# Optimization experiments

Measured on AMD Instinct MI355X. Metric: run time of the kernel, lower is better.

## Reference

```python
import jax, jax.numpy as jnp
import numpy as np

N_NODES = 50000
N_EDGES = 1000000


def _edge_conv(x, src, dst, W, b, n_nodes):
    """PyG EdgeConv: msg = nn(cat([x_i, x_j - x_i])), aggr=max over incoming edges."""
    xi = x[dst]                      # [E, C] target features
    xj = x[src]                      # [E, C] source features
    m = jnp.concatenate([xi, xj - xi], axis=-1)          # [E, 2C]
    m = jax.nn.relu(m @ W + b)                           # [E, C_out]
    out = jax.ops.segment_max(m, dst, num_segments=n_nodes)  # [N, C_out]
    # empty segments produce -inf; PyG fills with 0
    return jnp.where(jnp.isfinite(out), out, 0.0)


def setup_inputs() -> dict:
    key = jax.random.key(0)
    ks = jax.random.split(key, 12)
    x = jax.random.normal(ks[0], (N_NODES, 3), dtype=jnp.float32)
    edge_index = jax.random.randint(ks[1], (2, N_EDGES), 0, N_NODES, dtype=jnp.int64)

    def lin(k, fan_in, fan_out):
        s = 1.0 / np.sqrt(fan_in)
        kw, kb = jax.random.split(k)
        W = jax.random.uniform(kw, (fan_in, fan_out), jnp.float32, -s, s)
        b = jax.random.uniform(kb, (fan_out,), jnp.float32, -s, s)
        return W, b

    W1, b1 = lin(ks[2], 6, 64)       # conv1 MLP([3*2, 64])
    W2, b2 = lin(ks[3], 128, 128)    # conv2 MLP([64*2, 128])
    W3, b3 = lin(ks[4], 256, 512)    # conv3 MLP([128*2, 512])
    W4, b4 = lin(ks[5], 512, 256)    # lin1 MLP([512, 256])
    W5, b5 = lin(ks[6], 256, 3)      # lin1 final Linear(256, 3)
    return {"x": x, "edge_index": edge_index,
            "W1": W1, "b1": b1, "W2": W2, "b2": b2, "W3": W3, "b3": b3,
            "W4": W4, "b4": b4, "W5": W5, "b5": b5}


def reference(x, edge_index, W1, b1, W2, b2, W3, b3, W4, b4, W5, b5):
    src = edge_index[0]  # x_j
    dst = edge_index[1]  # x_i (aggregation target)
    n = x.shape[0]
    x1 = _edge_conv(x, src, dst, W1, b1, n)    # [N, 64]
    x2 = _edge_conv(x1, src, dst, W2, b2, n)   # [N, 128]
    x3 = _edge_conv(x2, src, dst, W3, b3, n)   # [N, 512]
    x4 = jax.nn.relu(x3 @ W4 + b4) @ W5 + b5   # [N, 3]
    return x + x4
```

## Files before the change

kernel.cpp:

```cpp
#include <hip/hip_runtime.h>

static constexpr int NN = 50000;
static constexpr int NE = 1000000;

typedef short bf16x8 __attribute__((ext_vector_type(8)));
typedef float f32x4 __attribute__((ext_vector_type(4)));
typedef unsigned short u16x2 __attribute__((ext_vector_type(2)));

__device__ inline float bf2f_raw(unsigned short u) {
    return __uint_as_float(((unsigned int)u) << 16);
}
__device__ inline unsigned short f2bf(float f) {
    unsigned int u = __float_as_uint(f);
    u += 0x7fffu + ((u >> 16) & 1u);
    return (unsigned short)(u >> 16);
}
__device__ inline unsigned short f2bfs(float f) {
    unsigned short b = f2bf(f);
    return (b & 0x8000u) ? (unsigned short)(~b) : (unsigned short)(b | 0x8000u);
}
__device__ inline float unsrt2f(unsigned short v) {
    unsigned short b = (v & 0x8000u) ? (unsigned short)(v ^ 0x8000u)
                                     : (unsigned short)(~v);
    return bf2f_raw(b);
}
__device__ inline unsigned int pkmax(unsigned int a, unsigned int b) {
    u16x2 r = __builtin_elementwise_max(__builtin_bit_cast(u16x2, a),
                                        __builtin_bit_cast(u16x2, b));
    return __builtin_bit_cast(unsigned int, r);
}
__device__ inline uint4 pkmax4(uint4 a, uint4 b) {
    a.x = pkmax(a.x, b.x); a.y = pkmax(a.y, b.y);
    a.z = pkmax(a.z, b.z); a.w = pkmax(a.w, b.w);
    return a;
}
__device__ inline unsigned int pack2(float f0, float f1) {
    return (unsigned int)f2bf(f0) | ((unsigned int)f2bf(f1) << 16);
}
__device__ inline unsigned int addrelu2t(unsigned int a, unsigned int t) {
    float t0 = unsrt2f((unsigned short)(t & 0xffffu));
    float t1 = unsrt2f((unsigned short)(t >> 16));
    float f0 = fmaxf(bf2f_raw((unsigned short)(a & 0xffffu)) + t0, 0.f);
    float f1 = fmaxf(bf2f_raw((unsigned short)(a >> 16)) + t1, 0.f);
    return pack2(f0, f1);
}


__global__ void setup_kernel(const float* __restrict__ x, const float* __restrict__ W1,
                             const float* __restrict__ b1, const float* __restrict__ b5,
                             const float* __restrict__ W2, const float* __restrict__ W3,
                             const float* __restrict__ W4,
                             unsigned short* __restrict__ as1, float* __restrict__ out,
                             int* __restrict__ deg, int* __restrict__ cursor,
                             unsigned short* __restrict__ Bt2,
                             unsigned short* __restrict__ Bt3,
                             unsigned short* __restrict__ W4t) {
    int t = blockIdx.x * blockDim.x + threadIdx.x;
    if (t < NN * 128) {
        int i = t >> 7, c = t & 127;
        float x0 = x[i * 3 + 0], x1 = x[i * 3 + 1], x2 = x[i * 3 + 2];
        if (c < 64) {
            float v = x0 * (W1[c] - W1[192 + c]) + x1 * (W1[64 + c] - W1[256 + c]) +
                      x2 * (W1[128 + c] - W1[320 + c]) + b1[c];
            as1[t] = f2bf(v);
        } else {
            int cs = c - 64;
            float v = x0 * W1[192 + cs] + x1 * W1[256 + cs] + x2 * W1[320 + cs];
            as1[t] = f2bfs(v);
        }
        return;
    }
    t -= NN * 128;
    if (t < NN * 3) { out[t] = x[t] + b5[t % 3]; return; }
    t -= NN * 3;
    if (t < NN) { deg[t] = 0; return; }
    t -= NN;
    if (t < NN) { cursor[t] = 0; return; }
    t -= NN;
    if (t < 8192) {
        int k = t / 128, c = t % 128;
        float wt = W2[k * 128 + c];
        float wb = W2[(64 + k) * 128 + c];
        Bt2[c * 64 + k] = f2bf(wt - wb);
        Bt2[(128 + c) * 64 + k] = f2bf(wb);
        return;
    }
    t -= 8192;
    if (t < 65536) {
        int k = t / 512, c = t % 512;
        float wt = W3[k * 512 + c];
        float wb = W3[(128 + k) * 512 + c];
        Bt3[c * 128 + k] = f2bf(wt - wb);
        Bt3[(512 + c) * 128 + k] = f2bf(wb);
        return;
    }
    t -= 65536;
    if (t < 131072) {
        int k = t / 256, n = t % 256;
        W4t[n * 512 + k] = f2bf(W4[k * 256 + n]);
    }
}


__global__ void hist_kernel(const int* __restrict__ dst, int* __restrict__ deg) {
    int e = blockIdx.x * blockDim.x + threadIdx.x;
    if (e < NE) atomicAdd(&deg[dst[e]], 1);
}

__global__ __launch_bounds__(1024) void scan_kernel(const int* __restrict__ deg,
                                                    int* __restrict__ rowstart) {
    __shared__ int wave_sums[16];
    constexpr int CH = (NN + 1023) / 1024;
    int tid = threadIdx.x;
    int lane = tid & 63;
    int wave = tid >> 6;
    int base = tid * CH;
    int vals[CH];
    int sum = 0;
    #pragma unroll
    for (int i = 0; i < CH; ++i) {
        int idx = base + i;
        vals[i] = (idx < NN) ? deg[idx] : 0;
        sum += vals[i];
    }
    int x = sum;
    #pragma unroll
    for (int off = 1; off < 64; off <<= 1) {
        int y = __shfl_up(x, off);
        if (lane >= off) x += y;
    }
    if (lane == 63) wave_sums[wave] = x;
    __syncthreads();
    if (wave == 0 && lane < 16) {
        int s = wave_sums[lane];
        #pragma unroll
        for (int off = 1; off < 16; off <<= 1) {
            int y = __shfl_up(s, off);
            if (lane >= off) s += y;
        }
        wave_sums[lane] = s;
    }
    __syncthreads();
    int run = (wave ? wave_sums[wave - 1] : 0) + x - sum;
    #pragma unroll
    for (int i = 0; i < CH; ++i) {
        int idx = base + i;
        if (idx < NN) rowstart[idx] = run;
        run += vals[i];
    }
    if (tid == 1023) rowstart[NN] = run;
}

__global__ void scatter_kernel(const int* __restrict__ src, const int* __restrict__ dst,
                               const int* __restrict__ rowstart, int* __restrict__ cursor,
                               int* __restrict__ csr) {
    int e = blockIdx.x * blockDim.x + threadIdx.x;
    if (e < NE) {
        int d = dst[e];
        int pos = atomicAdd(&cursor[d], 1);
        csr[rowstart[d] + pos] = src[e];
    }
}


__global__ __launch_bounds__(256) void edge_fused_conv1_kernel(
    const unsigned short* __restrict__ as, const int* __restrict__ rowstart,
    const int* __restrict__ csr, unsigned short* __restrict__ x1) {
    int wid = (blockIdx.x * 256 + threadIdx.x) >> 6;
    int lane = threadIdx.x & 63;
    if (wid >= NN) return;
    int e0 = __builtin_amdgcn_readfirstlane(rowstart[wid]);
    int e1 = __builtin_amdgcn_readfirstlane(rowstart[wid + 1]);
    int nedge = e1 - e0;
    unsigned int mA = 0u, mB = 0u;
    if (nedge > 0) {
        int last = nedge - 1;
        for (int e = 0; e < nedge; e += 16) {
            int jj[16];
            #pragma unroll
            for (int k = 0; k < 16; ++k) {
                int idx = e + k; if (idx > last) idx = last;
                jj[k] = __builtin_amdgcn_readfirstlane(csr[e0 + idx]);
            }
            unsigned int v[16];
            #pragma unroll
            for (int k = 0; k < 16; ++k)
                v[k] = *(const unsigned short*)(as + (size_t)jj[k] * 128 + 64 + lane);
            #pragma unroll
            for (int k = 0; k < 16; ++k) {
                if (k & 1) mB = mB > v[k] ? mB : v[k];
                else       mA = mA > v[k] ? mA : v[k];
            }
        }
    }
    unsigned int m = mA > mB ? mA : mB;
    unsigned short a = as[(size_t)wid * 128 + lane];
    float t = unsrt2f((unsigned short)m);
    float f = fmaxf(bf2f_raw(a) + t, 0.f);
    x1[(size_t)wid * 64 + lane] = f2bf(f);
}


__global__ __launch_bounds__(256) void ef128_a2_kernel(
    const unsigned short* __restrict__ s2, const unsigned short* __restrict__ x1,
    const int* __restrict__ rowstart, const int* __restrict__ csr,
    const unsigned short* __restrict__ Bt2a, const float* __restrict__ b2,
    unsigned short* __restrict__ x2) {
    __shared__ __align__(16) unsigned short x1t[16][72];
    __shared__ __align__(16) unsigned short A2[16][136];
    int tid = threadIdx.x;
    int wave = tid >> 6, lane = tid & 63;
    int quad = lane >> 4, l16 = lane & 15;
    int tilebase = blockIdx.x * 16;

    if (tid < 128) {
        int row = tid >> 3, seg = tid & 7;
        uint4 v = *(const uint4*)(x1 + (size_t)(tilebase + row) * 64 + seg * 8);
        *(uint4*)&x1t[row][seg * 8] = v;
    }
    __syncthreads();

    unsigned int m[4];
    for (int i = 0; i < 4; ++i) {
        int node = tilebase + wave * 4 + i;
        int e0 = __builtin_amdgcn_readfirstlane(rowstart[node]);
        int e1 = __builtin_amdgcn_readfirstlane(rowstart[node + 1]);
        int nedge = e1 - e0;
        unsigned int mA = 0u, mB = 0u;
        if (nedge > 0) {
            int last = nedge - 1;
            for (int e = 0; e < nedge; e += 16) {
                int jj[16];
                #pragma unroll
                for (int k = 0; k < 16; ++k) {
                    int idx = e + k; if (idx > last) idx = last;
                    jj[k] = __builtin_amdgcn_readfirstlane(csr[e0 + idx]);
                }
                unsigned int v[16];
                #pragma unroll
                for (int k = 0; k < 16; ++k)
                    v[k] = *(const unsigned int*)(s2 + (size_t)jj[k] * 128 + lane * 2);
                #pragma unroll
                for (int k = 0; k < 16; ++k) {
                    if (k & 1) mB = pkmax(mB, v[k]);
                    else       mA = pkmax(mA, v[k]);
                }
            }
        }
        m[i] = pkmax(mA, mB);
    }

    {
        int colbase = wave * 32;
        f32x4 acc[2] = {};
        #pragma unroll
        for (int kc = 0; kc < 2; ++kc) {
            bf16x8 afr = *(const bf16x8*)&x1t[l16][kc * 32 + quad * 8];
            #pragma unroll
            for (int nt = 0; nt < 2; ++nt) {
                int col = colbase + nt * 16 + l16;
                bf16x8 bfr = *(const bf16x8*)&Bt2a[(size_t)col * 64 + kc * 32 + quad * 8];
                acc[nt] = __builtin_amdgcn_mfma_f32_16x16x32_bf16(afr, bfr, acc[nt], 0, 0, 0);
            }
        }
        #pragma unroll
        for (int nt = 0; nt < 2; ++nt) {
            int col = colbase + nt * 16 + l16;
            float bv = b2[col];
            #pragma unroll
            for (int r = 0; r < 4; ++r)
                A2[quad * 4 + r][col] = f2bf(acc[nt][r] + bv);
        }
    }
    __syncthreads();

    #pragma unroll
    for (int i = 0; i < 4; ++i) {
        int row = wave * 4 + i;
        unsigned int av = *(const unsigned int*)&A2[row][lane * 2];
        *(unsigned int*)(x2 + (size_t)(tilebase + row) * 128 + lane * 2) =
            addrelu2t(av, m[i]);
    }
}


__global__ __launch_bounds__(256) void ef512_w5_kernel(
    const unsigned short* __restrict__ s3, const unsigned short* __restrict__ x2,
    const int* __restrict__ rowstart, const int* __restrict__ csr,
    const unsigned short* __restrict__ Bt3a, const float* __restrict__ b3,
    const unsigned short* __restrict__ W4t,
    const float* __restrict__ b4, const float* __restrict__ W5,
    float* __restrict__ out) {
    __shared__ __align__(16) unsigned short X[16][520];
    int tid = threadIdx.x;
    int wave = tid >> 6, lane = tid & 63;
    int quad = lane >> 4, l16 = lane & 15;
    int tilebase = blockIdx.x * 16;

    {
        int row = tid >> 4, seg = tid & 15;
        uint4 v = *(const uint4*)(x2 + (size_t)(tilebase + row) * 128 + seg * 8);
        *(uint4*)&X[row][seg * 8] = v;
    }
    __syncthreads();
    bf16x8 afr[4];
    #pragma unroll
    for (int kc = 0; kc < 4; ++kc)
        afr[kc] = *(const bf16x8*)&X[l16][kc * 32 + quad * 8];
    __syncthreads();

    uint4 m[4];
    for (int i = 0; i < 4; ++i) {
        int node = tilebase + wave * 4 + i;
        int e0 = __builtin_amdgcn_readfirstlane(rowstart[node]);
        int e1 = __builtin_amdgcn_readfirstlane(rowstart[node + 1]);
        int nedge = e1 - e0;
        uint4 mA = make_uint4(0u, 0u, 0u, 0u), mB = make_uint4(0u, 0u, 0u, 0u);
        if (nedge > 0) {
            int last = nedge - 1;
            for (int e = 0; e < nedge; e += 8) {
                int jj[8];
                #pragma unroll
                for (int k = 0; k < 8; ++k) {
                    int idx = e + k; if (idx > last) idx = last;
                    jj[k] = __builtin_amdgcn_readfirstlane(csr[e0 + idx]);
                }
                uint4 v[8];
                #pragma unroll
                for (int k = 0; k < 8; ++k)
                    v[k] = *(const uint4*)(s3 + (size_t)jj[k] * 512 + lane * 8);
                #pragma unroll
                for (int k = 0; k < 8; ++k) {
                    if (k & 1) mB = pkmax4(mB, v[k]);
                    else       mA = pkmax4(mA, v[k]);
                }
            }
        }
        m[i] = pkmax4(mA, mB);
    }

    {
        int colbase = wave * 128;
        f32x4 acc3[8] = {};
        #pragma unroll
        for (int kc = 0; kc < 4; ++kc) {
            #pragma unroll
            for (int nt = 0; nt < 8; ++nt) {
                int col = colbase + nt * 16 + l16;
                bf16x8 bfr = *(const bf16x8*)&Bt3a[(size_t)col * 128 + kc * 32 + quad * 8];
                acc3[nt] = __builtin_amdgcn_mfma_f32_16x16x32_bf16(afr[kc], bfr, acc3[nt], 0, 0, 0);
            }
        }
        #pragma unroll
        for (int nt = 0; nt < 8; ++nt) {
            int col = colbase + nt * 16 + l16;
            float bv = b3[col];
            #pragma unroll
            for (int r = 0; r < 4; ++r)
                X[quad * 4 + r][col] = f2bf(acc3[nt][r] + bv);
        }
    }
    __syncthreads();

    #pragma unroll
    for (int i = 0; i < 4; ++i) {
        int row = wave * 4 + i;
        uint4 av = *(const uint4*)&X[row][lane * 8];
        uint4 o;
        o.x = addrelu2t(av.x, m[i].x);
        o.y = addrelu2t(av.y, m[i].y);
        o.z = addrelu2t(av.z, m[i].z);
        o.w = addrelu2t(av.w, m[i].w);
        *(uint4*)&X[row][lane * 8] = o;
    }
    __syncthreads();

    int colbase = wave * 64;
    f32x4 acc4[4] = {};
    for (int kc = 0; kc < 16; ++kc) {
        bf16x8 a4 = *(const bf16x8*)&X[l16][kc * 32 + quad * 8];
        #pragma unroll
        for (int nt = 0; nt < 4; ++nt) {
            int col = colbase + nt * 16 + l16;
            bf16x8 bfr = *(const bf16x8*)&W4t[(size_t)col * 512 + kc * 32 + quad * 8];
            acc4[nt] = __builtin_amdgcn_mfma_f32_16x16x32_bf16(a4, bfr, acc4[nt], 0, 0, 0);
        }
    }
    float b4v[4], w5r[4][3];
    #pragma unroll
    for (int nt = 0; nt < 4; ++nt) {
        int col = colbase + nt * 16 + l16;
        b4v[nt] = b4[col];
        w5r[nt][0] = W5[col * 3 + 0];
        w5r[nt][1] = W5[col * 3 + 1];
        w5r[nt][2] = W5[col * 3 + 2];
    }
    #pragma unroll
    for (int r = 0; r < 4; ++r) {
        int row = tilebase + quad * 4 + r;
        float p0 = 0.f, p1 = 0.f, p2 = 0.f;
        #pragma unroll
        for (int nt = 0; nt < 4; ++nt) {
            float h = fmaxf(acc4[nt][r] + b4v[nt], 0.f);
            p0 += h * w5r[nt][0];
            p1 += h * w5r[nt][1];
            p2 += h * w5r[nt][2];
        }
        #pragma unroll
        for (int mm = 8; mm; mm >>= 1) {
            p0 += __shfl_xor(p0, mm);
            p1 += __shfl_xor(p1, mm);
            p2 += __shfl_xor(p2, mm);
        }
        if (l16 == 0) {
            atomicAdd(&out[row * 3 + 0], p0);
            atomicAdd(&out[row * 3 + 1], p1);
            atomicAdd(&out[row * 3 + 2], p2);
        }
    }
}


template<int K, int NT>
__global__ __launch_bounds__(256) void mfma_gemm_nloop_kernel(
    const unsigned short* __restrict__ A, const unsigned short* __restrict__ Bt,
    const float* __restrict__ bias, int bias_n,
    unsigned short* __restrict__ C, int M) {
    constexpr int KC = K / 32;
    constexpr int N = NT * 128;
    __shared__ __align__(16) unsigned short Asl[KC][128 * 40];
    __shared__ __align__(16) unsigned short Bsl[128 * 40];
    int tid = threadIdx.x;
    int mbase = blockIdx.x * 128;
    int wave = tid >> 6, lane = tid & 63;
    int wm = (wave >> 1) * 64, wn = (wave & 1) * 64;
    int quad = lane >> 4, l16 = lane & 15;

    #pragma unroll
    for (int c = tid; c < KC * 512; c += 256) {
        int kc = c >> 9, rem = c & 511;
        int r = rem >> 2, kk = (rem & 3) * 8;
        uint4 va = make_uint4(0u, 0u, 0u, 0u);
        int gr = mbase + r;
        if (gr < M) va = *(const uint4*)&A[(size_t)gr * K + kc * 32 + kk];
        *(uint4*)&Asl[kc][r * 40 + kk] = va;
    }

    for (int nt = 0; nt < NT; ++nt) {
        int nbase = nt * 128;
        f32x4 acc[4][4] = {};
        for (int kc = 0; kc < KC; ++kc) {
            __syncthreads();
            #pragma unroll
            for (int h = 0; h < 2; ++h) {
                int c = tid + h * 256;
                int r = c >> 2, kk = (c & 3) * 8;
                uint4 vb = *(const uint4*)&Bt[(size_t)(nbase + r) * K + kc * 32 + kk];
                *(uint4*)&Bsl[r * 40 + kk] = vb;
            }
            __syncthreads();
            bf16x8 af[4], bfr[4];
            #pragma unroll
            for (int tt = 0; tt < 4; ++tt) {
                af[tt]  = *(const bf16x8*)&Asl[kc][(wm + tt * 16 + l16) * 40 + quad * 8];
                bfr[tt] = *(const bf16x8*)&Bsl[(wn + tt * 16 + l16) * 40 + quad * 8];
            }
            #pragma unroll
            for (int mt = 0; mt < 4; ++mt)
                #pragma unroll
                for (int ntt = 0; ntt < 4; ++ntt)
                    acc[mt][ntt] = __builtin_amdgcn_mfma_f32_16x16x32_bf16(
                        af[mt], bfr[ntt], acc[mt][ntt], 0, 0, 0);
        }
        #pragma unroll
        for (int mt = 0; mt < 4; ++mt) {
            #pragma unroll
            for (int r = 0; r < 4; ++r) {
                int row = mbase + wm + mt * 16 + quad * 4 + r;
                if (row >= M) continue;
                #pragma unroll
                for (int ntt = 0; ntt < 4; ++ntt) {
                    int col = nbase + wn + ntt * 16 + l16;
                    float v = acc[mt][ntt][r];
                    unsigned short o;
                    if (col < bias_n) o = f2bf(v + bias[col]);
                    else o = f2bfs(v);
                    C[(size_t)row * N + col] = o;
                }
            }
        }
    }
}

__global__ void fallback_copy_kernel(const float* __restrict__ x, float* __restrict__ out) {
    int t = blockIdx.x * blockDim.x + threadIdx.x;
    if (t < NN * 3) out[t] = x[t];
}


extern "C" void kernel_launch(void* const* d_in, const int* in_sizes, int n_in,
                              void* d_out, int out_size, void* d_ws, size_t ws_size,
                              hipStream_t stream) {
    const float* x  = (const float*)d_in[0];
    const int*   ei = (const int*)d_in[1];
    const float* W1 = (const float*)d_in[2];
    const float* b1 = (const float*)d_in[3];
    const float* W2 = (const float*)d_in[4];
    const float* b2 = (const float*)d_in[5];
    const float* W3 = (const float*)d_in[6];
    const float* b3 = (const float*)d_in[7];
    const float* W4 = (const float*)d_in[8];
    const float* b4 = (const float*)d_in[9];
    const float* W5 = (const float*)d_in[10];
    const float* b5 = (const float*)d_in[11];
    float* out = (float*)d_out;

    char* p = (char*)d_ws;
    auto alloc = [&](size_t bytes) -> void* {
        void* r = (void*)p;
        p += (bytes + 255) & ~(size_t)255;
        return r;
    };
    int* deg      = (int*)alloc((size_t)NN * 4);
    int* rowstart = (int*)alloc((size_t)(NN + 1) * 4);
    int* cursor   = (int*)alloc((size_t)NN * 4);
    int* csr      = (int*)alloc((size_t)NE * 4);
    unsigned short* Bt2 = (unsigned short*)alloc(256 * 64 * 2);
    unsigned short* Bt3 = (unsigned short*)alloc(1024 * 128 * 2);
    unsigned short* W4t = (unsigned short*)alloc(256 * 512 * 2);
    unsigned short* x1 = (unsigned short*)alloc((size_t)NN * 64 * 2);
    unsigned short* x2 = (unsigned short*)alloc((size_t)NN * 128 * 2);
    unsigned short* as_slab = (unsigned short*)alloc((size_t)NN * 512 * 2);
    size_t need = (size_t)(p - (char*)d_ws);
    if (ws_size < need) {
        fallback_copy_kernel<<<(NN * 3 + 255) / 256, 256, 0, stream>>>(x, out);
        return;
    }

    const int* src = ei;
    const int* dst = ei + NE;

    constexpr int SETUP_T = NN * 128 + NN * 3 + NN + NN + 8192 + 65536 + 131072;
    setup_kernel<<<(SETUP_T + 255) / 256, 256, 0, stream>>>(
        x, W1, b1, b5, W2, W3, W4, as_slab, out, deg, cursor, Bt2, Bt3, W4t);

    hist_kernel<<<(NE + 255) / 256, 256, 0, stream>>>(dst, deg);
    scan_kernel<<<1, 1024, 0, stream>>>(deg, rowstart);
    scatter_kernel<<<(NE + 255) / 256, 256, 0, stream>>>(src, dst, rowstart, cursor, csr);

    edge_fused_conv1_kernel<<<12500, 256, 0, stream>>>(as_slab, rowstart, csr, x1);

    mfma_gemm_nloop_kernel<64, 1><<<391, 256, 0, stream>>>(
        x1, Bt2 + 128 * 64, b2, 0, as_slab, NN);
    ef128_a2_kernel<<<NN / 16, 256, 0, stream>>>(
        as_slab, x1, rowstart, csr, Bt2, b2, x2);

    mfma_gemm_nloop_kernel<128, 4><<<391, 256, 0, stream>>>(
        x2, Bt3 + 512 * 128, b3, 0, as_slab, NN);

    ef512_w5_kernel<<<NN / 16, 256, 0, stream>>>(
        as_slab, x2, rowstart, csr, Bt3, b3, W4t, b4, W5, out);
}
```

Baseline: 579.0 us.

## Compute per-edge source transforms on the fly for conv1 and conv2

Conv1 no longer precomputes a per-node source-transform slab. Each wave loads the raw 3-float coordinates of its neighbours, shares them via shuffles, and evaluates the 3-term dot product inline. Conv2 drops its separate source GEMM kernel: it gathers 64-wide x1 neighbour rows into shared memory, runs MFMA per 16-edge batch, and max-reduces into a shared sortable-bf16 buffer. This trades the slab writes and gather bandwidth for recomputed per-edge GEMMs (16x more MFMA work in conv2) and extra LDS traffic. The conv3 kernel also moves its self-GEMM ahead of the neighbour gather.

```diff
diff --git a/kernel.cpp b/kernel.cpp
--- a/kernel.cpp
+++ b/kernel.cpp
@@ -50,27 +50,21 @@
                              const float* __restrict__ b1, const float* __restrict__ b5,
                              const float* __restrict__ W2, const float* __restrict__ W3,
                              const float* __restrict__ W4,
-                             unsigned short* __restrict__ as1, float* __restrict__ out,
+                             unsigned short* __restrict__ a1buf, float* __restrict__ out,
                              int* __restrict__ deg, int* __restrict__ cursor,
                              unsigned short* __restrict__ Bt2,
                              unsigned short* __restrict__ Bt3,
                              unsigned short* __restrict__ W4t) {
     int t = blockIdx.x * blockDim.x + threadIdx.x;
-    if (t < NN * 128) {
-        int i = t >> 7, c = t & 127;
+    if (t < NN * 64) {
+        int i = t >> 6, c = t & 63;
         float x0 = x[i * 3 + 0], x1 = x[i * 3 + 1], x2 = x[i * 3 + 2];
-        if (c < 64) {
-            float v = x0 * (W1[c] - W1[192 + c]) + x1 * (W1[64 + c] - W1[256 + c]) +
-                      x2 * (W1[128 + c] - W1[320 + c]) + b1[c];
-            as1[t] = f2bf(v);
-        } else {
-            int cs = c - 64;
-            float v = x0 * W1[192 + cs] + x1 * W1[256 + cs] + x2 * W1[320 + cs];
-            as1[t] = f2bfs(v);
-        }
+        float v = x0 * (W1[c] - W1[192 + c]) + x1 * (W1[64 + c] - W1[256 + c]) +
+                  x2 * (W1[128 + c] - W1[320 + c]) + b1[c];
+        a1buf[t] = f2bf(v);
         return;
     }
-    t -= NN * 128;
+    t -= NN * 64;
     if (t < NN * 3) { out[t] = x[t] + b5[t % 3]; return; }
     t -= NN * 3;
     if (t < NN) { deg[t] = 0; return; }
@@ -163,51 +157,50 @@
 }
 
 
-__global__ __launch_bounds__(256) void edge_fused_conv1_kernel(
-    const unsigned short* __restrict__ as, const int* __restrict__ rowstart,
-    const int* __restrict__ csr, unsigned short* __restrict__ x1) {
+__global__ __launch_bounds__(256) void conv1_kernel(
+    const float* __restrict__ x, const int* __restrict__ rowstart,
+    const int* __restrict__ csr, const float* __restrict__ W1,
+    const unsigned short* __restrict__ a1buf, unsigned short* __restrict__ x1) {
     int wid = (blockIdx.x * 256 + threadIdx.x) >> 6;
     int lane = threadIdx.x & 63;
     if (wid >= NN) return;
     int e0 = __builtin_amdgcn_readfirstlane(rowstart[wid]);
     int e1 = __builtin_amdgcn_readfirstlane(rowstart[wid + 1]);
-    int nedge = e1 - e0;
-    unsigned int mA = 0u, mB = 0u;
-    if (nedge > 0) {
-        int last = nedge - 1;
-        for (int e = 0; e < nedge; e += 16) {
-            int jj[16];
+    int ne = e1 - e0;
+    float wa = W1[192 + lane], wb = W1[256 + lane], wc = W1[320 + lane];
+    float m = -INFINITY;
+    if (ne > 0) {
+        int last = ne - 1;
+        int eidx = lane >> 2, comp = lane & 3;
+        for (int e = 0; e < ne; e += 16) {
+            int idx = e + eidx; if (idx > last) idx = last;
+            int j = csr[e0 + idx];
+            float v = 0.f;
+            if (comp < 3) v = x[(size_t)j * 3 + comp];
             #pragma unroll
             for (int k = 0; k < 16; ++k) {
-                int idx = e + k; if (idx > last) idx = last;
-                jj[k] = __builtin_amdgcn_readfirstlane(csr[e0 + idx]);
-            }
-            unsigned int v[16];
-            #pragma unroll
-            for (int k = 0; k < 16; ++k)
-                v[k] = *(const unsigned short*)(as + (size_t)jj[k] * 128 + 64 + lane);
-            #pragma unroll
-            for (int k = 0; k < 16; ++k) {
-                if (k & 1) mB = mB > v[k] ? mB : v[k];
-                else       mA = mA > v[k] ? mA : v[k];
-            }
-        }
-    }
-    unsigned int m = mA > mB ? mA : mB;
-    unsigned short a = as[(size_t)wid * 128 + lane];
-    float t = unsrt2f((unsigned short)m);
-    float f = fmaxf(bf2f_raw(a) + t, 0.f);
-    x1[(size_t)wid * 64 + lane] = f2bf(f);
-}
-
-
-__global__ __launch_bounds__(256) void ef128_a2_kernel(
-    const unsigned short* __restrict__ s2, const unsigned short* __restrict__ x1,
-    const int* __restrict__ rowstart, const int* __restrict__ csr,
-    const unsigned short* __restrict__ Bt2a, const float* __restrict__ b2,
-    unsigned short* __restrict__ x2) {
+                float x0 = __shfl(v, k * 4 + 0);
+                float x1v = __shfl(v, k * 4 + 1);
+                float x2v = __shfl(v, k * 4 + 2);
+                float s = x0 * wa + x1v * wb + x2v * wc;
+                s = bf2f_raw(f2bf(s));
+                m = fmaxf(m, s);
+            }
+        }
+    }
+    float a = bf2f_raw(a1buf[(size_t)wid * 64 + lane]);
+    x1[(size_t)wid * 64 + lane] = f2bf(fmaxf(a + m, 0.f));
+}
+
+
+__global__ __launch_bounds__(256) void ef128_x1_kernel(
+    const unsigned short* __restrict__ x1, const int* __restrict__ rowstart,
+    const int* __restrict__ csr, const unsigned short* __restrict__ Bt2,
+    const float* __restrict__ b2, unsigned short* __restrict__ x2) {
     __shared__ __align__(16) unsigned short x1t[16][72];
     __shared__ __align__(16) unsigned short A2[16][136];
+    __shared__ __align__(16) unsigned short M[16][136];
+    __shared__ __align__(16) unsigned short E[4][16][72];
     int tid = threadIdx.x;
     int wave = tid >> 6, lane = tid & 63;
     int quad = lane >> 4, l16 = lane & 15;
@@ -218,37 +211,12 @@
         uint4 v = *(const uint4*)(x1 + (size_t)(tilebase + row) * 64 + seg * 8);
         *(uint4*)&x1t[row][seg * 8] = v;
     }
-    __syncthreads();
-
-    unsigned int m[4];
-    for (int i = 0; i < 4; ++i) {
-        int node = tilebase + wave * 4 + i;
-        int e0 = __builtin_amdgcn_readfirstlane(rowstart[node]);
-        int e1 = __builtin_amdgcn_readfirstlane(rowstart[node + 1]);
-        int nedge = e1 - e0;
-        unsigned int mA = 0u, mB = 0u;
-        if (nedge > 0) {
-            int last = nedge - 1;
-            for (int e = 0; e < nedge; e += 16) {
-                int jj[16];
-                #pragma unroll
-                for (int k = 0; k < 16; ++k) {
-                    int idx = e + k; if (idx > last) idx = last;
-                    jj[k] = __builtin_amdgcn_readfirstlane(csr[e0 + idx]);
-                }
-                unsigned int v[16];
-                #pragma unroll
-                for (int k = 0; k < 16; ++k)
-                    v[k] = *(const unsigned int*)(s2 + (size_t)jj[k] * 128 + lane * 2);
-                #pragma unroll
-                for (int k = 0; k < 16; ++k) {
-                    if (k & 1) mB = pkmax(mB, v[k]);
-                    else       mA = pkmax(mA, v[k]);
-                }
-            }
-        }
-        m[i] = pkmax(mA, mB);
-    }
+    #pragma unroll
+    for (int idx = tid; idx < 16 * 64; idx += 256) {
+        int row = idx >> 6, c2 = idx & 63;
+        *(unsigned int*)&M[row][c2 * 2] = 0u;
+    }
+    __syncthreads();
 
     {
         int colbase = wave * 32;
@@ -259,7 +227,7 @@
             #pragma unroll
             for (int nt = 0; nt < 2; ++nt) {
                 int col = colbase + nt * 16 + l16;
-                bf16x8 bfr = *(const bf16x8*)&Bt2a[(size_t)col * 64 + kc * 32 + quad * 8];
+                bf16x8 bfr = *(const bf16x8*)&Bt2[(size_t)col * 64 + kc * 32 + quad * 8];
                 acc[nt] = __builtin_amdgcn_mfma_f32_16x16x32_bf16(afr, bfr, acc[nt], 0, 0, 0);
             }
         }
@@ -272,14 +240,68 @@
                 A2[quad * 4 + r][col] = f2bf(acc[nt][r] + bv);
         }
     }
+
+    for (int i = 0; i < 4; ++i) {
+        int nl = wave * 4 + i;
+        int node = tilebase + nl;
+        int e0 = __builtin_amdgcn_readfirstlane(rowstart[node]);
+        int e1 = __builtin_amdgcn_readfirstlane(rowstart[node + 1]);
+        int ne = e1 - e0;
+        if (ne <= 0) continue;
+        int last = ne - 1;
+        for (int e = 0; e < ne; e += 16) {
+            int cj[8];
+            #pragma unroll
+            for (int sub = 0; sub < 8; ++sub) {
+                int ee = sub * 2 + (lane >> 5);
+                int idx = e + ee; if (idx > last) idx = last;
+                cj[sub] = csr[e0 + idx];
+            }
+            unsigned int g[8];
+            #pragma unroll
+            for (int sub = 0; sub < 8; ++sub)
+                g[sub] = *(const unsigned int*)(x1 + (size_t)cj[sub] * 64 + (lane & 31) * 2);
+            #pragma unroll
+            for (int sub = 0; sub < 8; ++sub)
+                *(unsigned int*)&E[wave][sub * 2 + (lane >> 5)][(lane & 31) * 2] = g[sub];
+            #pragma unroll
+            for (int half = 0; half < 2; ++half) {
+                f32x4 acc[4] = {};
+                #pragma unroll
+                for (int kc = 0; kc < 2; ++kc) {
+                    bf16x8 afr = *(const bf16x8*)&E[wave][l16][kc * 32 + quad * 8];
+                    #pragma unroll
+                    for (int nt = 0; nt < 4; ++nt) {
+                        int col = half * 64 + nt * 16 + l16;
+                        bf16x8 bfr = *(const bf16x8*)&Bt2[(size_t)(128 + col) * 64 + kc * 32 + quad * 8];
+                        acc[nt] = __builtin_amdgcn_mfma_f32_16x16x32_bf16(afr, bfr, acc[nt], 0, 0, 0);
+                    }
+                }
+                #pragma unroll
+                for (int nt = 0; nt < 4; ++nt) {
+                    float cm = fmaxf(fmaxf(acc[nt][0], acc[nt][1]),
+                                     fmaxf(acc[nt][2], acc[nt][3]));
+                    cm = fmaxf(cm, __shfl_xor(cm, 16));
+                    cm = fmaxf(cm, __shfl_xor(cm, 32));
+                    if (lane < 16) {
+                        unsigned short sv = f2bfs(cm);
+                        int col = half * 64 + nt * 16 + l16;
+                        unsigned short old = M[nl][col];
+                        if (sv > old) M[nl][col] = sv;
+                    }
+                }
+            }
+        }
+    }
     __syncthreads();
 
     #pragma unroll
     for (int i = 0; i < 4; ++i) {
         int row = wave * 4 + i;
         unsigned int av = *(const unsigned int*)&A2[row][lane * 2];
+        unsigned int mv = *(const unsigned int*)&M[row][lane * 2];
         *(unsigned int*)(x2 + (size_t)(tilebase + row) * 128 + lane * 2) =
-            addrelu2t(av, m[i]);
+            addrelu2t(av, mv);
     }
 }
 
@@ -309,6 +331,28 @@
         afr[kc] = *(const bf16x8*)&X[l16][kc * 32 + quad * 8];
     __syncthreads();
 
+    {
+        int colbase = wave * 128;
+        f32x4 acc3[8] = {};
+        #pragma unroll
+        for (int kc = 0; kc < 4; ++kc) {
+            #pragma unroll
+            for (int nt = 0; nt < 8; ++nt) {
+                int col = colbase + nt * 16 + l16;
+                bf16x8 bfr = *(const bf16x8*)&Bt3a[(size_t)col * 128 + kc * 32 + quad * 8];
+                acc3[nt] = __builtin_amdgcn_mfma_f32_16x16x32_bf16(afr[kc], bfr, acc3[nt], 0, 0, 0);
+            }
+        }
+        #pragma unroll
+        for (int nt = 0; nt < 8; ++nt) {
+            int col = colbase + nt * 16 + l16;
+            float bv = b3[col];
+            #pragma unroll
+            for (int r = 0; r < 4; ++r)
+                X[quad * 4 + r][col] = f2bf(acc3[nt][r] + bv);
+        }
+    }
+
     uint4 m[4];
     for (int i = 0; i < 4; ++i) {
         int node = tilebase + wave * 4 + i;
@@ -337,28 +381,6 @@
             }
         }
         m[i] = pkmax4(mA, mB);
-    }
-
-    {
-        int colbase = wave * 128;
-        f32x4 acc3[8] = {};
-        #pragma unroll
-        for (int kc = 0; kc < 4; ++kc) {
-            #pragma unroll
-            for (int nt = 0; nt < 8; ++nt) {
-                int col = colbase + nt * 16 + l16;
-                bf16x8 bfr = *(const bf16x8*)&Bt3a[(size_t)col * 128 + kc * 32 + quad * 8];
-                acc3[nt] = __builtin_amdgcn_mfma_f32_16x16x32_bf16(afr[kc], bfr, acc3[nt], 0, 0, 0);
-            }
-        }
-        #pragma unroll
-        for (int nt = 0; nt < 8; ++nt) {
-            int col = colbase + nt * 16 + l16;
-            float bv = b3[col];
-            #pragma unroll
-            for (int r = 0; r < 4; ++r)
-                X[quad * 4 + r][col] = f2bf(acc3[nt][r] + bv);
-        }
     }
     __syncthreads();
 
@@ -528,9 +550,10 @@
     unsigned short* Bt2 = (unsigned short*)alloc(256 * 64 * 2);
     unsigned short* Bt3 = (unsigned short*)alloc(1024 * 128 * 2);
     unsigned short* W4t = (unsigned short*)alloc(256 * 512 * 2);
+    unsigned short* a1 = (unsigned short*)alloc((size_t)NN * 64 * 2);
     unsigned short* x1 = (unsigned short*)alloc((size_t)NN * 64 * 2);
     unsigned short* x2 = (unsigned short*)alloc((size_t)NN * 128 * 2);
-    unsigned short* as_slab = (unsigned short*)alloc((size_t)NN * 512 * 2);
+    unsigned short* s3 = (unsigned short*)alloc((size_t)NN * 512 * 2);
     size_t need = (size_t)(p - (char*)d_ws);
     if (ws_size < need) {
         fallback_copy_kernel<<<(NN * 3 + 255) / 256, 256, 0, stream>>>(x, out);
@@ -540,24 +563,21 @@
     const int* src = ei;
     const int* dst = ei + NE;
 
-    constexpr int SETUP_T = NN * 128 + NN * 3 + NN + NN + 8192 + 65536 + 131072;
+    constexpr int SETUP_T = NN * 64 + NN * 3 + NN + NN + 8192 + 65536 + 131072;
     setup_kernel<<<(SETUP_T + 255) / 256, 256, 0, stream>>>(
-        x, W1, b1, b5, W2, W3, W4, as_slab, out, deg, cursor, Bt2, Bt3, W4t);
+        x, W1, b1, b5, W2, W3, W4, a1, out, deg, cursor, Bt2, Bt3, W4t);
 
     hist_kernel<<<(NE + 255) / 256, 256, 0, stream>>>(dst, deg);
     scan_kernel<<<1, 1024, 0, stream>>>(deg, rowstart);
     scatter_kernel<<<(NE + 255) / 256, 256, 0, stream>>>(src, dst, rowstart, cursor, csr);
 
-    edge_fused_conv1_kernel<<<12500, 256, 0, stream>>>(as_slab, rowstart, csr, x1);
-
-    mfma_gemm_nloop_kernel<64, 1><<<391, 256, 0, stream>>>(
-        x1, Bt2 + 128 * 64, b2, 0, as_slab, NN);
-    ef128_a2_kernel<<<NN / 16, 256, 0, stream>>>(
-        as_slab, x1, rowstart, csr, Bt2, b2, x2);
+    conv1_kernel<<<12500, 256, 0, stream>>>(x, rowstart, csr, W1, a1, x1);
+
+    ef128_x1_kernel<<<NN / 16, 256, 0, stream>>>(x1, rowstart, csr, Bt2, b2, x2);
 
     mfma_gemm_nloop_kernel<128, 4><<<391, 256, 0, stream>>>(
-        x2, Bt3 + 512 * 128, b3, 0, as_slab, NN);
+        x2, Bt3 + 512 * 128, b3, 0, s3, NN);
 
     ef512_w5_kernel<<<NN / 16, 256, 0, stream>>>(
-        as_slab, x2, rowstart, csr, Bt3, b3, W4t, b4, W5, out);
-}
+        s3, x2, rowstart, csr, Bt3, b3, W4t, b4, W5, out);
+}
```

Result: slower. 670.6 us (+15.8%).
